# Kernel tuning notes

Hardware: AMD Instinct MI355X
Metric: run time of the kernel (lower is better)

## Reference

```python
import jax, jax.numpy as jnp
from jax import lax
import numpy as np

EPS_START, EPS_END, EPS_DECAY = 1.0, 0.05, 10000.0


def gru_step(x, h, w_ih, w_hh, b_ih, b_hh):
    # PyTorch GRUCell math; gates stacked as [r, z, n]
    gi = x @ w_ih.T + b_ih
    gh = h @ w_hh.T + b_hh
    i_r, i_z, i_n = jnp.split(gi, 3, axis=1)
    h_r, h_z, h_n = jnp.split(gh, 3, axis=1)
    r = jax.nn.sigmoid(i_r + h_r)
    z = jax.nn.sigmoid(i_z + h_z)
    n = jnp.tanh(i_n + r * h_n)
    return (1.0 - z) * n + z * h


def setup_inputs() -> dict:
    key = jax.random.key(0)
    ks = jax.random.split(key, 7)
    V, E, H = 32000, 256, 512
    s = 0.05
    return {
        "embedding": jax.random.normal(ks[0], (V, E), jnp.float32) * s,
        "w_ih": jax.random.normal(ks[1], (3 * H, E), jnp.float32) * s,
        "w_hh": jax.random.normal(ks[2], (3 * H, H), jnp.float32) * s,
        "b_ih": jax.random.normal(ks[3], (3 * H,), jnp.float32) * s,
        "b_hh": jax.random.normal(ks[4], (3 * H,), jnp.float32) * s,
        "w_out": jax.random.normal(ks[5], (V, H), jnp.float32) * s,
        "b_out": jax.random.normal(ks[6], (V,), jnp.float32) * s,
        "seq_len": 256,
        "batch_size": 512,
    }


def reference(embedding, w_ih, w_hh, b_ih, b_hh, w_out, b_out, seq_len, batch_size):
    V, E = embedding.shape
    H = w_hh.shape[1]
    B = batch_size
    log_unif = jnp.float32(np.log(V))  # -log(vocab_size) fill for epsilon-greedy

    keys = jax.random.split(jax.random.key(42), seq_len)
    ts = jnp.arange(seq_len, dtype=jnp.float32)

    h0 = jnp.zeros((B, H), jnp.float32)
    x0 = jnp.broadcast_to(embedding[0], (B, E))  # start token id 0

    def step(carry, inp):
        h, x = carry
        t, k = inp
        k_eps, k_gum = jax.random.split(k)
        h = gru_step(x, h, w_ih, w_hh, b_ih, b_hh)
        logp = jax.nn.log_softmax(h @ w_out.T + b_out, axis=1)  # [B, V]
        eps_t = EPS_END + (EPS_START - EPS_END) * jnp.exp(-4.0 * t / EPS_DECAY)
        draw = eps_t >= jax.random.uniform(k_eps, (B,))
        masked = jnp.where(draw[:, None], -log_unif, logp)
        g = jax.random.gumbel(k_gum, (B, V), jnp.float32)
        sampled = jnp.argmax(masked + g, axis=1)  # [B] int
        lp = jnp.take_along_axis(logp, sampled[:, None], axis=1)[:, 0]
        x_next = embedding[sampled]
        return (h, x_next), (sampled, lp)

    _, (samples, lps) = lax.scan(step, (h0, x0), (ts, keys))
    return samples.T, lps.T  # [B, S] each
```

## Files before the change

### kernel.cpp

```cpp
#include <hip/hip_runtime.h>
#include <math.h>
#include <stdio.h>

#ifndef JAX_PARTITIONABLE
#define JAX_PARTITIONABLE 1
#endif

namespace {

constexpr int B  = 512;
constexpr int S  = 256;
constexpr int E  = 256;
constexpr int H  = 512;
constexpr int V  = 32000;
constexpr int G3 = 3 * H;
constexpr int VBLK = 64;
constexpr int NCH  = V / VBLK;
constexpr int NDMAX = 96;

typedef __bf16 bf16x8 __attribute__((ext_vector_type(8)));
typedef float  f32x4  __attribute__((ext_vector_type(4)));
typedef unsigned u32x4 __attribute__((ext_vector_type(4)));

__device__ __forceinline__ void tf2x32(unsigned k0, unsigned k1,
                                       unsigned x0, unsigned x1,
                                       unsigned& o0, unsigned& o1) {
  unsigned ks2 = k0 ^ k1 ^ 0x1BD11BDAu;
  x0 += k0; x1 += k1;
#define TFR(r) { x0 += x1; x1 = (x1 << (r)) | (x1 >> (32 - (r))); x1 ^= x0; }
  TFR(13) TFR(15) TFR(26) TFR(6)   x0 += k1;  x1 += ks2 + 1u;
  TFR(17) TFR(29) TFR(16) TFR(24)  x0 += ks2; x1 += k0 + 2u;
  TFR(13) TFR(15) TFR(26) TFR(6)   x0 += k0;  x1 += k1 + 3u;
  TFR(17) TFR(29) TFR(16) TFR(24)  x0 += k1;  x1 += ks2 + 4u;
  TFR(13) TFR(15) TFR(26) TFR(6)   x0 += ks2; x1 += k0 + 5u;
#undef TFR
  o0 = x0; o1 = x1;
}

__device__ __forceinline__ unsigned rbits(unsigned g0, unsigned g1,
                                          unsigned b, unsigned v) {
#if JAX_PARTITIONABLE
  unsigned y0, y1;
  tf2x32(g0, g1, 0u, b * (unsigned)V + v, y0, y1);
  return y0 ^ y1;
#else
  const unsigned N2 = (unsigned)(B/2) * (unsigned)V;
  unsigned ii = b * (unsigned)V + v;
  unsigned jj = (b < 256) ? ii : ii - N2;
  unsigned y0, y1;
  tf2x32(g0, g1, jj, N2 + jj, y0, y1);
  return (b < 256) ? y0 : y1;
#endif
}

__device__ __forceinline__ float u01_from_bits(unsigned bits) {
  return __uint_as_float(0x3f800000u | (bits >> 9)) - 1.0f;
}

__device__ __forceinline__ float gumbel_exact(unsigned bits) {
  float u = u01_from_bits(bits);
  if (u == 0.0f) u = 1.1754943508222875e-38f;
  float w = (float)(-log((double)u));
  return (float)(-log((double)w));
}

__device__ __forceinline__ float gumbel_fast(unsigned bits) {
  float u = u01_from_bits(bits);
  if (u == 0.0f) u = 1.1754943508222875e-38f;
  float w = -__logf(u);
  return -__logf(w);
}

__device__ __forceinline__ unsigned short f2bf(float f) {
  unsigned u = __float_as_uint(f);
  unsigned r = (u + 0x7fffu + ((u >> 16) & 1u)) >> 16;
  return (unsigned short)r;
}

__device__ __forceinline__ size_t frag_off(int row, int k, int kTiles) {
  return ((size_t)((row >> 4) * kTiles + (k >> 5)) * 64
          + (row & 15) + 16 * ((k >> 3) & 3)) * 8 + (k & 7);
}

__global__ void k_init_rng(unsigned* __restrict__ kq, unsigned* __restrict__ ke) {
  int t = threadIdx.x;
  unsigned h0, h1, e0, e1, g0, g1;
#if JAX_PARTITIONABLE
  tf2x32(0u, 42u, 0u, (unsigned)t, h0, h1);
  tf2x32(h0, h1, 0u, 0u, e0, e1);
  tf2x32(h0, h1, 0u, 1u, g0, g1);
#else
  unsigned a0, a1, b0, b1;
  if (t < 128) {
    tf2x32(0u, 42u, (unsigned)(2*t),   (unsigned)(256+2*t), a0, a1);
    tf2x32(0u, 42u, (unsigned)(2*t+1), (unsigned)(257+2*t), b0, b1);
    h0 = a0; h1 = b0;
  } else {
    int j = 2*t - 256;
    tf2x32(0u, 42u, (unsigned)j,     (unsigned)(256+j), a0, a1);
    tf2x32(0u, 42u, (unsigned)(j+1), (unsigned)(257+j), b0, b1);
    h0 = a1; h1 = b1;
  }
  unsigned p0, p1, q0, q1;
  tf2x32(h0, h1, 0u, 2u, p0, p1);
  tf2x32(h0, h1, 1u, 3u, q0, q1);
  e0 = p0; e1 = q0; g0 = p1; g1 = q1;
#endif
  ke[2*t] = e0; ke[2*t+1] = e1;
  kq[2*t] = g0; kq[2*t+1] = g1;
}

__global__ void k_init_draws(const unsigned* __restrict__ ke,
                             unsigned char* __restrict__ draws) {
  int t = blockIdx.x;
  int b = threadIdx.x;
  unsigned k0 = ke[2*t], k1 = ke[2*t+1];
  unsigned bits, y0, y1;
#if JAX_PARTITIONABLE
  tf2x32(k0, k1, 0u, (unsigned)b, y0, y1);
  bits = y0 ^ y1;
#else
  if (b < 256) { tf2x32(k0, k1, (unsigned)b,       (unsigned)(256+b), y0, y1); bits = y0; }
  else         { tf2x32(k0, k1, (unsigned)(b-256), (unsigned)b,       y0, y1); bits = y1; }
#endif
  float u   = u01_from_bits(bits);
  float tf  = (float)t;
  float ex  = expf(__fmul_rn(-4.0f, tf) / 10000.0f);
  float eps = __fadd_rn(0.05f, __fmul_rn(0.95f, ex));
  draws[t*B + b] = (eps >= u) ? 1 : 0;
}

__global__ void k_init_nd(const unsigned char* __restrict__ draws,
                          int* __restrict__ nd_slot) {
  int t = blockIdx.x;
  if (threadIdx.x != 0) return;
  int cnt = 0;
  for (int b = 0; b < B; b++) {
    if (!draws[t*B + b] && cnt < NDMAX) nd_slot[t*B + b] = cnt++;
    else nd_slot[t*B + b] = -1;
  }
}

__global__ __launch_bounds__(256) void k_pre_argmax(
    const unsigned* __restrict__ kq, const unsigned char* __restrict__ draws,
    int* __restrict__ pre) {
  const int job  = blockIdx.x * 4 + (threadIdx.x >> 6);
  const int lane = threadIdx.x & 63;
  const int t = job >> 9, b = job & (B - 1);
  if (!draws[t*B + b]) { if (lane == 0) pre[job] = -1; return; }
  const unsigned g0 = kq[2*t], g1 = kq[2*t+1];
  unsigned best = 0u; int bv = V;
  for (int v = lane; v < V; v += 64) {
    unsigned bits = rbits(g0, g1, (unsigned)b, (unsigned)v) >> 9;
    if (bits > best || (bits == best && v < bv)) { best = bits; bv = v; }
  }
#pragma unroll
  for (int m = 1; m < 64; m <<= 1) {
    unsigned ob = __shfl_xor(best, m, 64);
    int      ov = __shfl_xor(bv,   m, 64);
    if (ob > best || (ob == best && ov < bv)) { best = ob; bv = ov; }
  }
  if (lane == 0) pre[job] = bv;
}

__global__ void k_init_state(float* __restrict__ h, int* __restrict__ samp) {
  int b = blockIdx.x, tid = threadIdx.x;
  h[b*H + tid] = 0.0f;
  h[b*H + 256 + tid] = 0.0f;
  if (tid == 0) samp[b] = 0;
}

__global__ void k_cast_w(const float* __restrict__ w,
                         unsigned short* __restrict__ w_sw) {
  int g = blockIdx.x*256 + threadIdx.x;
  int v  = g >> 6;
  int k0 = (g & 63) * 8;
  const float* src = w + (size_t)v*H + k0;
  union { unsigned short s[8]; u32x4 vv; } u;
#pragma unroll
  for (int e = 0; e < 8; e++) u.s[e] = f2bf(src[e]);
  *(u32x4*)&w_sw[frag_off(v, k0, H/32)] = u.vv;
}

__global__ __launch_bounds__(512) void k_emb_gates(
    const float* __restrict__ emb, const float* __restrict__ w_ih,
    const float* __restrict__ b_ih, float* __restrict__ EG) {
  __shared__ __align__(16) float As[16][68];
  __shared__ __align__(16) float Ws[16][68];
  const int tid = threadIdx.x;
  const int tx = tid & 15, ty = tid >> 4;
  const int row0 = blockIdx.y * 64, col0 = blockIdx.x * 64;
  float acc[2][4] = {};
  for (int k0 = 0; k0 < E; k0 += 16) {
#pragma unroll
    for (int l = 0; l < 2; l++) {
      int idx = tid + l*512;
      int r = idx >> 4, kk = idx & 15;
      As[kk][r] = emb[(size_t)(row0 + r)*E + k0 + kk];
      Ws[kk][r] = w_ih[(size_t)(col0 + r)*E + k0 + kk];
    }
    __syncthreads();
#pragma unroll
    for (int kk = 0; kk < 16; kk++) {
      const float2 av = *(const float2*)&As[kk][ty*2];
      const float4 wv = *(const float4*)&Ws[kk][tx*4];
      const float a[2] = {av.x, av.y};
      const float w[4] = {wv.x, wv.y, wv.z, wv.w};
#pragma unroll
      for (int i = 0; i < 2; i++)
#pragma unroll
        for (int j = 0; j < 4; j++) acc[i][j] = fmaf(a[i], w[j], acc[i][j]);
    }
    __syncthreads();
  }
#pragma unroll
  for (int i = 0; i < 2; i++) {
    int r = row0 + ty*2 + i;
    int c = col0 + tx*4;
    float4 o;
    o.x = __fadd_rn(acc[i][0], b_ih[c + 0]);
    o.y = __fadd_rn(acc[i][1], b_ih[c + 1]);
    o.z = __fadd_rn(acc[i][2], b_ih[c + 2]);
    o.w = __fadd_rn(acc[i][3], b_ih[c + 3]);
    *(float4*)&EG[(size_t)r*G3 + c] = o;
  }
}

__device__ __forceinline__ float sigm_acc(float v) {
  return (float)(1.0 / (1.0 + exp(-(double)v)));
}
__device__ __forceinline__ float tanh_acc(float v) {
  return (float)tanh((double)v);
}

__global__ __launch_bounds__(256) void k_gates_finish(
    const float* __restrict__ h, const float* __restrict__ w_hh,
    const float* __restrict__ b_hh, float* __restrict__ gh,
    const float* __restrict__ pmax, const float* __restrict__ psum,
    const float* __restrict__ plog,
    int* __restrict__ pre, const int* __restrict__ nd_slot,
    const float* __restrict__ nd_keys, const float* __restrict__ nd_kmax,
    const unsigned* __restrict__ kq, const unsigned char* __restrict__ draws,
    const float* __restrict__ w_out, const float* __restrict__ b_out,
    float* __restrict__ out_samples, float* __restrict__ out_lps,
    int* __restrict__ samp, int t) {
  const int tid = threadIdx.x;
  union Sh {
    struct { float As[2][16][68]; float Ws[2][16][52]; } g;
    struct { float sA[256]; int cand[160]; float ck[160]; float cl[160];
             int ccnt; int samp; float blog; } f;
    struct { unsigned sb[4]; int sv[4]; } p;
  };
  __shared__ Sh sh;

  if (blockIdx.x < 256) {
    if (t >= S) return;
    const int jw = tid & 15, rg = tid >> 4;
    const int j0 = (blockIdx.x & 31) * 16;
    const int row0 = (blockIdx.x >> 5) * 64;
    float ah[4][3] = {};
    float pa[4], pw[3];
#pragma unroll
    for (int l = 0; l < 4; l++) {
      int idx = tid + l*256;
      pa[l] = h[(size_t)(row0 + (idx >> 4))*H + (idx & 15)];
    }
#pragma unroll
    for (int l = 0; l < 3; l++) {
      int idx = tid + l*256;
      int c = idx >> 4;
      pw[l] = w_hh[(size_t)((c >> 4)*512 + j0 + (c & 15))*H + (idx & 15)];
    }
#pragma unroll
    for (int l = 0; l < 4; l++) {
      int idx = tid + l*256;
      sh.g.As[0][idx & 15][idx >> 4] = pa[l];
    }
#pragma unroll
    for (int l = 0; l < 3; l++) {
      int idx = tid + l*256;
      sh.g.Ws[0][idx & 15][idx >> 4] = pw[l];
    }
    __syncthreads();
    int p = 0;
#pragma unroll 1
    for (int tile = 0; tile < 32; tile++) {
      if (tile < 31) {
        const int k0 = (tile + 1) * 16;
#pragma unroll
        for (int l = 0; l < 4; l++) {
          int idx = tid + l*256;
          pa[l] = h[(size_t)(row0 + (idx >> 4))*H + k0 + (idx & 15)];
        }
#pragma unroll
        for (int l = 0; l < 3; l++) {
          int idx = tid + l*256;
          int c = idx >> 4;
          pw[l] = w_hh[(size_t)((c >> 4)*512 + j0 + (c & 15))*H + k0 + (idx & 15)];
        }
      }
#pragma unroll
      for (int kk = 0; kk < 16; kk++) {
        const float4 av = *(const float4*)&sh.g.As[p][kk][rg*4];
        const float a[4] = {av.x, av.y, av.z, av.w};
        const float w0 = sh.g.Ws[p][kk][jw];
        const float w1 = sh.g.Ws[p][kk][16 + jw];
        const float w2 = sh.g.Ws[p][kk][32 + jw];
#pragma unroll
        for (int i = 0; i < 4; i++) {
          ah[i][0] = fmaf(a[i], w0, ah[i][0]);
          ah[i][1] = fmaf(a[i], w1, ah[i][1]);
          ah[i][2] = fmaf(a[i], w2, ah[i][2]);
        }
      }
      if (tile < 31) {
#pragma unroll
        for (int l = 0; l < 4; l++) {
          int idx = tid + l*256;
          sh.g.As[p ^ 1][idx & 15][idx >> 4] = pa[l];
        }
#pragma unroll
        for (int l = 0; l < 3; l++) {
          int idx = tid + l*256;
          sh.g.Ws[p ^ 1][idx & 15][idx >> 4] = pw[l];
        }
        __syncthreads();
        p ^= 1;
      }
    }
    const int j = j0 + jw;
    const float bh_r = b_hh[j], bh_z = b_hh[512 + j], bh_n = b_hh[1024 + j];
#pragma unroll
    for (int i = 0; i < 4; i++) {
      const int b = row0 + rg*4 + i;
      gh[(size_t)b*G3 +        j] = __fadd_rn(ah[i][0], bh_r);
      gh[(size_t)b*G3 +  512 + j] = __fadd_rn(ah[i][1], bh_z);
      gh[(size_t)b*G3 + 1024 + j] = __fadd_rn(ah[i][2], bh_n);
    }
    return;
  }

  if (blockIdx.x >= 768) {
    const int tn = t + 1;
    if (tn >= S) return;
    const int b = blockIdx.x - 768;
    if (!draws[tn*B + b]) { if (tid == 0) pre[tn*B + b] = -1; return; }
    const unsigned g0 = kq[2*tn], g1 = kq[2*tn+1];
    unsigned best = 0u; int bv = V;
    for (int v = tid; v < V; v += 256) {
      unsigned bits = rbits(g0, g1, (unsigned)b, (unsigned)v) >> 9;
      if (bits > best || (bits == best && v < bv)) { best = bits; bv = v; }
    }
#pragma unroll
    for (int m = 1; m < 64; m <<= 1) {
      unsigned ob = __shfl_xor(best, m, 64);
      int      ov = __shfl_xor(bv,   m, 64);
      if (ob > best || (ob == best && ov < bv)) { best = ob; bv = ov; }
    }
    const int wv = tid >> 6;
    if ((tid & 63) == 0) { sh.p.sb[wv] = best; sh.p.sv[wv] = bv; }
    __syncthreads();
    if (tid == 0) {
      for (int i = 1; i < 4; i++) {
        unsigned ob = sh.p.sb[i]; int ov = sh.p.sv[i];
        if (ob > best || (ob == best && ov < bv)) { best = ob; bv = ov; }
      }
      pre[tn*B + b] = bv;
    }
    return;
  }

  const int tf = t - 1;
  if (tf < 0) return;
  const int b = blockIdx.x - 256;
  const int* pre_t     = pre + tf*B;
  const int* nd_slot_t = nd_slot + tf*B;

  float m = -INFINITY;
  for (int c = tid; c < NCH; c += 256) m = fmaxf(m, pmax[b*NCH + c]);
  sh.f.sA[tid] = m; __syncthreads();
  for (int s = 128; s > 0; s >>= 1) {
    if (tid < s) sh.f.sA[tid] = fmaxf(sh.f.sA[tid], sh.f.sA[tid+s]);
    __syncthreads();
  }
  const float M = sh.f.sA[0];
  __syncthreads();
  float sum = 0.0f;
  for (int c = tid; c < NCH; c += 256)
    sum += psum[b*NCH + c] * expf(pmax[b*NCH + c] - M);
  sh.f.sA[tid] = sum; __syncthreads();
  for (int s = 128; s > 0; s >>= 1) {
    if (tid < s) sh.f.sA[tid] += sh.f.sA[tid+s];
    __syncthreads();
  }
  const float SUM = sh.f.sA[0];
  __syncthreads();

  const int pr = pre_t[b];
  if (pr >= 0) {
    if (tid == 0) { sh.f.samp = pr; sh.f.blog = plog[b]; }
  } else {
    const int slot = nd_slot_t[b];
    if (slot < 0) {
      if (tid == 0) { sh.f.samp = 0; sh.f.blog = plog[b]; }
    } else {
      const unsigned g0 = kq[2*tf], g1 = kq[2*tf+1];
      if (tid == 0) sh.f.ccnt = 0;
      float km = -INFINITY;
      for (int c = tid; c < NCH; c += 256) km = fmaxf(km, nd_kmax[slot*NCH + c]);
      sh.f.sA[tid] = km; __syncthreads();
      for (int s = 128; s > 0; s >>= 1) {
        if (tid < s) sh.f.sA[tid] = fmaxf(sh.f.sA[tid], sh.f.sA[tid+s]);
        __syncthreads();
      }
      const float thr = sh.f.sA[0] - 0.0859375f;
      __syncthreads();
      const float* keys = nd_keys + (size_t)slot*V;
      for (int c = tid; c < NCH; c += 256) {
        if (nd_kmax[slot*NCH + c] >= thr) {
          for (int j = 0; j < VBLK; j++) {
            float k = keys[c*VBLK + j];
            if (k >= thr) {
              int p = atomicAdd(&sh.f.ccnt, 1);
              if (p < 160) sh.f.cand[p] = c*VBLK + j;
            }
          }
        }
      }
      __syncthreads();
      const int nc = min(sh.f.ccnt, 160);
      const int wid = tid >> 6, lane = tid & 63;
      for (int c = wid; c < nc; c += 4) {
        const int v = sh.f.cand[c];
        const float* wr = w_out + (size_t)v*H;
        const float* hr = h + (size_t)b*H;
        float s = 0.0f;
#pragma unroll
        for (int i = 0; i < 8; i++) s = fmaf(hr[lane + 64*i], wr[lane + 64*i], s);
#pragma unroll
        for (int mm = 1; mm < 64; mm <<= 1) s += __shfl_xor(s, mm, 64);
        if (lane == 0) {
          float logit = __fadd_rn(s, b_out[v]);
          float key   = __fadd_rn(logit,
                          gumbel_exact(rbits(g0, g1, (unsigned)b, (unsigned)v)));
          sh.f.ck[c] = key; sh.f.cl[c] = logit;
        }
      }
      __syncthreads();
      if (tid == 0) {
        float bk = -INFINITY; int bv = V; float bl = 0.0f;
        for (int c = 0; c < nc; c++) {
          float k = sh.f.ck[c]; int v = sh.f.cand[c];
          if (k > bk || (k == bk && v < bv)) { bk = k; bv = v; bl = sh.f.cl[c]; }
        }
        sh.f.samp = bv; sh.f.blog = bl;
      }
    }
  }
  __syncthreads();
  if (tid == 0) {
    const int sampled = sh.f.samp;
    float lse = (float)log((double)SUM);
    float lp  = __fsub_rn(__fsub_rn(sh.f.blog, M), lse);
    out_samples[b*S + tf] = (float)sampled;
    out_lps[b*S + tf]     = lp;
    samp[b] = sampled;
  }
}

__global__ void k_gru(const float* __restrict__ EG, const int* __restrict__ samp,
                      const float* __restrict__ gh, float* __restrict__ h,
                      unsigned short* __restrict__ h_sw) {
  int g = blockIdx.x*256 + threadIdx.x;
  int b  = g >> 6;
  int j0 = (g & 63) * 8;
  const float* gib = EG + (size_t)samp[b]*G3;
  const float* ghb = gh + (size_t)b*G3;
  float hn[8];
  union { unsigned short s[8]; u32x4 vv; } u;
#pragma unroll
  for (int e = 0; e < 8; e++) {
    int j = j0 + e;
    float r  = sigm_acc(__fadd_rn(gib[j],     ghb[j]));
    float zz = sigm_acc(__fadd_rn(gib[H+j],   ghb[H+j]));
    float nn = tanh_acc(__fadd_rn(gib[2*H+j], __fmul_rn(r, ghb[2*H+j])));
    float hv = h[(size_t)b*H + j];
    float t1 = __fmul_rn(__fsub_rn(1.0f, zz), nn);
    float t2 = __fmul_rn(zz, hv);
    hn[e] = __fadd_rn(t1, t2);
    u.s[e] = f2bf(hn[e]);
  }
#pragma unroll
  for (int e = 0; e < 8; e++) h[(size_t)b*H + j0 + e] = hn[e];
  *(u32x4*)&h_sw[frag_off(b, j0, H/32)] = u.vv;
}

__global__ __launch_bounds__(256) void k_xgru(
    const float* __restrict__ emb, const int* __restrict__ samp,
    const float* __restrict__ w_ih, const float* __restrict__ b_ih,
    const float* __restrict__ gh, float* __restrict__ h,
    unsigned short* __restrict__ h_sw) {
  __shared__ __align__(16) float As[2][16][68];
  __shared__ __align__(16) float Ws[2][16][52];
  __shared__ int srow[64];
  const int tid = threadIdx.x;
  const int jw = tid & 15, rg = tid >> 4;
  const int j0 = blockIdx.x * 16;
  const int row0 = blockIdx.y * 64;
  if (tid < 64) srow[tid] = samp[row0 + tid];
  __syncthreads();

  float ai[4][3] = {};
  float pa[4], pw[3];
#pragma unroll
  for (int l = 0; l < 4; l++) {
    int idx = tid + l*256;
    pa[l] = emb[(size_t)srow[idx >> 4]*E + (idx & 15)];
  }
#pragma unroll
  for (int l = 0; l < 3; l++) {
    int idx = tid + l*256;
    int c = idx >> 4;
    pw[l] = w_ih[(size_t)((c >> 4)*512 + j0 + (c & 15))*E + (idx & 15)];
  }
#pragma unroll
  for (int l = 0; l < 4; l++) {
    int idx = tid + l*256;
    As[0][idx & 15][idx >> 4] = pa[l];
  }
#pragma unroll
  for (int l = 0; l < 3; l++) {
    int idx = tid + l*256;
    Ws[0][idx & 15][idx >> 4] = pw[l];
  }
  __syncthreads();
  int p = 0;
#pragma unroll 1
  for (int tile = 0; tile < 16; tile++) {
    if (tile < 15) {
      const int k0 = (tile + 1) * 16;
#pragma unroll
      for (int l = 0; l < 4; l++) {
        int idx = tid + l*256;
        pa[l] = emb[(size_t)srow[idx >> 4]*E + k0 + (idx & 15)];
      }
#pragma unroll
      for (int l = 0; l < 3; l++) {
        int idx = tid + l*256;
        int c = idx >> 4;
        pw[l] = w_ih[(size_t)((c >> 4)*512 + j0 + (c & 15))*E + k0 + (idx & 15)];
      }
    }
#pragma unroll
    for (int kk = 0; kk < 16; kk++) {
      const float4 av = *(const float4*)&As[p][kk][rg*4];
      const float a[4] = {av.x, av.y, av.z, av.w};
      const float w0 = Ws[p][kk][jw];
      const float w1 = Ws[p][kk][16 + jw];
      const float w2 = Ws[p][kk][32 + jw];
#pragma unroll
      for (int i = 0; i < 4; i++) {
        ai[i][0] = fmaf(a[i], w0, ai[i][0]);
        ai[i][1] = fmaf(a[i], w1, ai[i][1]);
        ai[i][2] = fmaf(a[i], w2, ai[i][2]);
      }
    }
    if (tile < 15) {
#pragma unroll
      for (int l = 0; l < 4; l++) {
        int idx = tid + l*256;
        As[p ^ 1][idx & 15][idx >> 4] = pa[l];
      }
#pragma unroll
      for (int l = 0; l < 3; l++) {
        int idx = tid + l*256;
        Ws[p ^ 1][idx & 15][idx >> 4] = pw[l];
      }
      __syncthreads();
      p ^= 1;
    }
  }

  const int j = j0 + jw;
  const float bi_r = b_ih[j], bi_z = b_ih[512 + j], bi_n = b_ih[1024 + j];
#pragma unroll
  for (int i = 0; i < 4; i++) {
    const int b = row0 + rg*4 + i;
    float gi_r = __fadd_rn(ai[i][0], bi_r);
    float gi_z = __fadd_rn(ai[i][1], bi_z);
    float gi_n = __fadd_rn(ai[i][2], bi_n);
    float gh_r = gh[(size_t)b*G3 + j];
    float gh_z = gh[(size_t)b*G3 + 512 + j];
    float gh_n = gh[(size_t)b*G3 + 1024 + j];
    float r  = sigm_acc(__fadd_rn(gi_r, gh_r));
    float zz = sigm_acc(__fadd_rn(gi_z, gh_z));
    float nn = tanh_acc(__fadd_rn(gi_n, __fmul_rn(r, gh_n)));
    float hv = h[(size_t)b*H + j];
    float t1 = __fmul_rn(__fsub_rn(1.0f, zz), nn);
    float t2 = __fmul_rn(zz, hv);
    float hn = __fadd_rn(t1, t2);
    h[(size_t)b*H + j] = hn;
    h_sw[frag_off(b, j, H/32)] = f2bf(hn);
  }
}

__global__ __launch_bounds__(256) void k_mfma_logits(
    const unsigned short* __restrict__ h_sw,
    const unsigned short* __restrict__ w_sw,
    const float* __restrict__ b_out,
    const unsigned* __restrict__ kq,
    const int* __restrict__ pre_t,
    const int* __restrict__ nd_slot_t,
    float* __restrict__ pmax, float* __restrict__ psum,
    float* __restrict__ plog,
    float* __restrict__ nd_keys, float* __restrict__ nd_kmax, int t) {
  const int tid  = threadIdx.x;

  const int L  = blockIdx.y * 512 + blockIdx.x;
  const int wg = (L & 7) * 128 + (L >> 3);
  if (wg >= 2*NCH) return;
  const int vblk = wg >> 1;
  const int bblk = wg & 1;
  const int lane = tid & 63, w = tid >> 6;
  const int quad = lane >> 4, l15 = lane & 15;

  f32x4 acc[4][4] = {};

  const int mtBase = bblk*16 + w*4;
  const int ntBase = vblk*4;
  const unsigned short* hp = h_sw + (size_t)mtBase*16*512 + lane*8;
  const unsigned short* wp = w_sw + (size_t)ntBase*16*512 + lane*8;

  bf16x8 afc[4], bfc[4];
#pragma unroll
  for (int mt = 0; mt < 4; mt++)
    afc[mt] = __builtin_bit_cast(bf16x8, *(const u32x4*)(hp + (size_t)(mt*16)*512));
#pragma unroll
  for (int nt = 0; nt < 4; nt++)
    bfc[nt] = __builtin_bit_cast(bf16x8, *(const u32x4*)(wp + (size_t)(nt*16)*512));

#pragma unroll 1
  for (int kt = 0; kt < 15; kt++) {
    bf16x8 afn[4], bfn[4];
#pragma unroll
    for (int mt = 0; mt < 4; mt++)
      afn[mt] = __builtin_bit_cast(bf16x8,
          *(const u32x4*)(hp + (size_t)(mt*16 + kt + 1)*512));
#pragma unroll
    for (int nt = 0; nt < 4; nt++)
      bfn[nt] = __builtin_bit_cast(bf16x8,
          *(const u32x4*)(wp + (size_t)(nt*16 + kt + 1)*512));
#pragma unroll
    for (int mt = 0; mt < 4; mt++)
#pragma unroll
      for (int nt = 0; nt < 4; nt++)
        acc[mt][nt] = __builtin_amdgcn_mfma_f32_16x16x32_bf16(
            afc[mt], bfc[nt], acc[mt][nt], 0, 0, 0);
#pragma unroll
    for (int mt = 0; mt < 4; mt++) afc[mt] = afn[mt];
#pragma unroll
    for (int nt = 0; nt < 4; nt++) bfc[nt] = bfn[nt];
  }
  {
#pragma unroll
    for (int mt = 0; mt < 4; mt++)
#pragma unroll
      for (int nt = 0; nt < 4; nt++)
        acc[mt][nt] = __builtin_amdgcn_mfma_f32_16x16x32_bf16(
            afc[mt], bfc[nt], acc[mt][nt], 0, 0, 0);
  }

  const int bW = bblk*256 + w*64;
  const int vW = vblk*64;
  const unsigned g0 = kq[2*t], g1 = kq[2*t+1];
  float bias[4];
#pragma unroll
  for (int nt = 0; nt < 4; nt++) bias[nt] = b_out[vW + nt*16 + l15];

#pragma unroll
  for (int mt = 0; mt < 4; mt++) {
#pragma unroll
    for (int r = 0; r < 4; r++) {
      const int b = bW + mt*16 + quad*4 + r;
      float lg[4];
#pragma unroll
      for (int nt = 0; nt < 4; nt++) lg[nt] = acc[mt][nt][r] + bias[nt];
      float lmax = fmaxf(fmaxf(lg[0], lg[1]), fmaxf(lg[2], lg[3]));
#pragma unroll
      for (int m = 1; m < 16; m <<= 1) lmax = fmaxf(lmax, __shfl_xor(lmax, m, 64));
      float ls = 0.0f;
#pragma unroll
      for (int nt = 0; nt < 4; nt++) ls += __expf(lg[nt] - lmax);
#pragma unroll
      for (int m = 1; m < 16; m <<= 1) ls += __shfl_xor(ls, m, 64);
      if (l15 == 0) { pmax[b*NCH + vblk] = lmax; psum[b*NCH + vblk] = ls; }
      const int pr = pre_t[b];
      if (pr >= 0) {
        int rel = pr - vW;
        if (rel >= 0 && rel < 64 && (rel & 15) == l15) plog[b] = lg[rel >> 4];
      } else {
        const int slot = nd_slot_t[b];
        if (slot >= 0) {
          float key[4];
#pragma unroll
          for (int nt = 0; nt < 4; nt++)
            key[nt] = lg[nt] + gumbel_fast(
                rbits(g0, g1, (unsigned)b, (unsigned)(vW + nt*16 + l15)));
          float* dst = nd_keys + (size_t)slot*V + vW + l15;
#pragma unroll
          for (int nt = 0; nt < 4; nt++) dst[nt*16] = key[nt];
          float kmx = fmaxf(fmaxf(key[0], key[1]), fmaxf(key[2], key[3]));
#pragma unroll
          for (int m = 1; m < 16; m <<= 1) kmx = fmaxf(kmx, __shfl_xor(kmx, m, 64));
          if (l15 == 0) nd_kmax[slot*NCH + vblk] = kmx;
        }
      }
    }
  }
}

}

extern "C" void kernel_launch(void* const* d_in, const int* in_sizes, int n_in,
                              void* d_out, int out_size, void* d_ws, size_t ws_size,
                              hipStream_t stream) {
  (void)in_sizes; (void)n_in; (void)out_size;
  const float* emb   = (const float*)d_in[0];
  const float* w_ih  = (const float*)d_in[1];
  const float* w_hh  = (const float*)d_in[2];
  const float* b_ih  = (const float*)d_in[3];
  const float* b_hh  = (const float*)d_in[4];
  const float* w_out = (const float*)d_in[5];
  const float* b_out = (const float*)d_in[6];
  float* out = (float*)d_out;

  char* wsb = (char*)d_ws;
  size_t off = 0;
  auto alloc = [&](size_t nbytes) {
    char* p = wsb + off;
    off += (nbytes + 255) & ~size_t(255);
    return p;
  };
  float* h     = (float*)alloc((size_t)B*H*4);
  float* gh    = (float*)alloc((size_t)B*G3*4);
  unsigned short* h_sw = (unsigned short*)alloc((size_t)B*H*2);
  unsigned short* w_sw = (unsigned short*)alloc((size_t)V*H*2);
  float* pmax  = (float*)alloc((size_t)B*NCH*4);
  float* psum  = (float*)alloc((size_t)B*NCH*4);
  float* plog  = (float*)alloc((size_t)B*4);
  unsigned* kq = (unsigned*)alloc((size_t)S*2*4);
  unsigned* ke = (unsigned*)alloc((size_t)S*2*4);
  unsigned char* draws = (unsigned char*)alloc((size_t)S*B);
  int* pre     = (int*)alloc((size_t)S*B*4);
  int* nd_slot = (int*)alloc((size_t)S*B*4);
  float* nd_keys = (float*)alloc((size_t)NDMAX*V*4);
  float* nd_kmax = (float*)alloc((size_t)NDMAX*NCH*4);
  int* samp    = (int*)alloc((size_t)B*4);
  if (off > ws_size) {
    fprintf(stderr, "kernel_launch: workspace too small (need %zu, have %zu)\n",
            off, ws_size);
    return;
  }
  const size_t eg_bytes = ((size_t)V*G3*4 + 255) & ~size_t(255);
  const bool use_eg = (off + eg_bytes <= ws_size);
  float* EG = use_eg ? (float*)alloc(eg_bytes) : nullptr;

  k_init_rng<<<1, S, 0, stream>>>(kq, ke);
  k_init_draws<<<S, B, 0, stream>>>(ke, draws);
  k_init_nd<<<S, 64, 0, stream>>>(draws, nd_slot);
  k_pre_argmax<<<B/4, 256, 0, stream>>>(kq, draws, pre);
  k_init_state<<<B, 256, 0, stream>>>(h, samp);
  k_cast_w<<<(V*H/8)/256, 256, 0, stream>>>(w_out, w_sw);
  if (use_eg)
    k_emb_gates<<<dim3(G3/64, V/64), 512, 0, stream>>>(emb, w_ih, b_ih, EG);

  for (int t = 0; t < S; t++) {
    k_gates_finish<<<1280, 256, 0, stream>>>(
        h, w_hh, b_hh, gh, pmax, psum, plog, pre, nd_slot,
        nd_keys, nd_kmax, kq, draws, w_out, b_out,
        out, out + (size_t)B*S, samp, t);
    if (use_eg)
      k_gru<<<(B*H/8)/256, 256, 0, stream>>>(EG, samp, gh, h, h_sw);
    else
      k_xgru<<<dim3(32, 8), 256, 0, stream>>>(emb, samp, w_ih, b_ih,
                                              gh, h, h_sw);
    k_mfma_logits<<<dim3(512, 2), 256, 0, stream>>>(
        h_sw, w_sw, b_out, kq, pre + t*B, nd_slot + t*B,
        pmax, psum, plog, nd_keys, nd_kmax, t);
  }
  k_gates_finish<<<1280, 256, 0, stream>>>(
      h, w_hh, b_hh, gh, pmax, psum, plog, pre, nd_slot,
      nd_keys, nd_kmax, kq, draws, w_out, b_out,
      out, out + (size_t)B*S, samp, S);
}
```

Baseline: 33.87 ms.

## Fuse sampling finish with GRU update and overlap hidden-gate GEMM with logits

Each step goes from three launches to two on the embedding-gate path. The new k_fingru combines finishing the previous step's sample with the GRU update. The recurrent h@w_hh GEMM for the next step now runs in extra blocks of the logits MFMA kernel, so it overlaps the output projection. The epsilon-branch argmax precompute is also moved from one upfront kernel into extra blocks of k_fingru. The aim is to cut per-step launch overhead and serial dependency, in exchange for more complex block-role dispatch, and gh is initialised to b_hh.

```diff
diff --git a/kernel.cpp b/kernel.cpp
--- a/kernel.cpp
+++ b/kernel.cpp
@@ -163,11 +163,15 @@
   if (lane == 0) pre[job] = bv;
 }
 
-__global__ void k_init_state(float* __restrict__ h, int* __restrict__ samp) {
+__global__ void k_init_state(float* __restrict__ h, int* __restrict__ samp,
+                             float* __restrict__ gh,
+                             const float* __restrict__ b_hh) {
   int b = blockIdx.x, tid = threadIdx.x;
   h[b*H + tid] = 0.0f;
   h[b*H + 256 + tid] = 0.0f;
   if (tid == 0) samp[b] = 0;
+#pragma unroll
+  for (int i = 0; i < 6; i++) gh[(size_t)b*G3 + i*256 + tid] = b_hh[i*256 + tid];
 }
 
 __global__ void k_cast_w(const float* __restrict__ w,
@@ -231,6 +235,382 @@
 }
 __device__ __forceinline__ float tanh_acc(float v) {
   return (float)tanh((double)v);
+}
+
+__global__ __launch_bounds__(256) void k_fingru(
+    const float* __restrict__ EG, const float* __restrict__ gh,
+    float* __restrict__ h, unsigned short* __restrict__ h_sw,
+    const float* __restrict__ pmax, const float* __restrict__ psum,
+    const float* __restrict__ plog,
+    int* __restrict__ pre, const int* __restrict__ nd_slot,
+    const float* __restrict__ nd_keys, const float* __restrict__ nd_kmax,
+    const unsigned* __restrict__ kq, const unsigned char* __restrict__ draws,
+    const float* __restrict__ w_out, const float* __restrict__ b_out,
+    float* __restrict__ out_samples, float* __restrict__ out_lps,
+    int* __restrict__ samp, int t) {
+  const int tid = threadIdx.x;
+
+  if (blockIdx.x >= 512) {
+    __shared__ unsigned sb[4];
+    __shared__ int      sv[4];
+    if (t >= S) return;
+    const int b = blockIdx.x - 512;
+    if (!draws[t*B + b]) { if (tid == 0) pre[t*B + b] = -1; return; }
+    const unsigned g0 = kq[2*t], g1 = kq[2*t+1];
+    unsigned best = 0u; int bv = V;
+    for (int v = tid; v < V; v += 256) {
+      unsigned bits = rbits(g0, g1, (unsigned)b, (unsigned)v) >> 9;
+      if (bits > best || (bits == best && v < bv)) { best = bits; bv = v; }
+    }
+#pragma unroll
+    for (int m = 1; m < 64; m <<= 1) {
+      unsigned ob = __shfl_xor(best, m, 64);
+      int      ov = __shfl_xor(bv,   m, 64);
+      if (ob > best || (ob == best && ov < bv)) { best = ob; bv = ov; }
+    }
+    const int wv = tid >> 6;
+    if ((tid & 63) == 0) { sb[wv] = best; sv[wv] = bv; }
+    __syncthreads();
+    if (tid == 0) {
+      for (int i = 1; i < 4; i++) {
+        unsigned ob = sb[i]; int ov = sv[i];
+        if (ob > best || (ob == best && ov < bv)) { best = ob; bv = ov; }
+      }
+      pre[t*B + b] = bv;
+    }
+    return;
+  }
+
+  const int b = blockIdx.x;
+  __shared__ float sA[256];
+  __shared__ int   cand[160];
+  __shared__ float cand_key[160], cand_lg[160];
+  __shared__ int   ccnt;
+  __shared__ int   s_samp;
+  __shared__ float s_blog;
+
+  const int tf = t - 1;
+  if (tf >= 0) {
+    const int* pre_t     = pre + tf*B;
+    const int* nd_slot_t = nd_slot + tf*B;
+
+    float m = -INFINITY;
+    for (int c = tid; c < NCH; c += 256) m = fmaxf(m, pmax[b*NCH + c]);
+    sA[tid] = m; __syncthreads();
+    for (int s = 128; s > 0; s >>= 1) {
+      if (tid < s) sA[tid] = fmaxf(sA[tid], sA[tid+s]);
+      __syncthreads();
+    }
+    const float M = sA[0];
+    __syncthreads();
+    float sum = 0.0f;
+    for (int c = tid; c < NCH; c += 256)
+      sum += psum[b*NCH + c] * expf(pmax[b*NCH + c] - M);
+    sA[tid] = sum; __syncthreads();
+    for (int s = 128; s > 0; s >>= 1) {
+      if (tid < s) sA[tid] += sA[tid+s];
+      __syncthreads();
+    }
+    const float SUM = sA[0];
+    __syncthreads();
+
+    const int pr = pre_t[b];
+    if (pr >= 0) {
+      if (tid == 0) { s_samp = pr; s_blog = plog[b]; }
+    } else {
+      const int slot = nd_slot_t[b];
+      if (slot < 0) {
+        if (tid == 0) { s_samp = 0; s_blog = plog[b]; }
+      } else {
+        const unsigned g0 = kq[2*tf], g1 = kq[2*tf+1];
+        if (tid == 0) ccnt = 0;
+        float km = -INFINITY;
+        for (int c = tid; c < NCH; c += 256) km = fmaxf(km, nd_kmax[slot*NCH + c]);
+        sA[tid] = km; __syncthreads();
+        for (int s = 128; s > 0; s >>= 1) {
+          if (tid < s) sA[tid] = fmaxf(sA[tid], sA[tid+s]);
+          __syncthreads();
+        }
+        const float thr = sA[0] - 0.0859375f;
+        __syncthreads();
+        const float* keys = nd_keys + (size_t)slot*V;
+        for (int c = tid; c < NCH; c += 256) {
+          if (nd_kmax[slot*NCH + c] >= thr) {
+            for (int j = 0; j < VBLK; j++) {
+              float k = keys[c*VBLK + j];
+              if (k >= thr) {
+                int p = atomicAdd(&ccnt, 1);
+                if (p < 160) cand[p] = c*VBLK + j;
+              }
+            }
+          }
+        }
+        __syncthreads();
+        const int nc = min(ccnt, 160);
+        const int wid = tid >> 6, lane = tid & 63;
+        for (int c = wid; c < nc; c += 4) {
+          const int v = cand[c];
+          const float* wr = w_out + (size_t)v*H;
+          const float* hr = h + (size_t)b*H;
+          float s = 0.0f;
+#pragma unroll
+          for (int i = 0; i < 8; i++) s = fmaf(hr[lane + 64*i], wr[lane + 64*i], s);
+#pragma unroll
+          for (int mm = 1; mm < 64; mm <<= 1) s += __shfl_xor(s, mm, 64);
+          if (lane == 0) {
+            float logit = __fadd_rn(s, b_out[v]);
+            float key   = __fadd_rn(logit,
+                            gumbel_exact(rbits(g0, g1, (unsigned)b, (unsigned)v)));
+            cand_key[c] = key; cand_lg[c] = logit;
+          }
+        }
+        __syncthreads();
+        if (tid == 0) {
+          float bk = -INFINITY; int bv = V; float bl = 0.0f;
+          for (int c = 0; c < nc; c++) {
+            float k = cand_key[c]; int v = cand[c];
+            if (k > bk || (k == bk && v < bv)) { bk = k; bv = v; bl = cand_lg[c]; }
+          }
+          s_samp = bv; s_blog = bl;
+        }
+      }
+    }
+    __syncthreads();
+    if (tid == 0) {
+      const int sampled = s_samp;
+      float lse = (float)log((double)SUM);
+      float lp  = __fsub_rn(__fsub_rn(s_blog, M), lse);
+      out_samples[b*S + tf] = (float)sampled;
+      out_lps[b*S + tf]     = lp;
+      samp[b] = sampled;
+    }
+    __syncthreads();
+  }
+
+  if (t >= S) return;
+  const int smp = (tf >= 0) ? s_samp : samp[b];
+
+  const float* gib = EG + (size_t)smp*G3;
+  const float* ghb = gh + (size_t)b*G3;
+#pragma unroll
+  for (int e = 0; e < 2; e++) {
+    const int j = tid*2 + e;
+    float r  = sigm_acc(__fadd_rn(gib[j],     ghb[j]));
+    float zz = sigm_acc(__fadd_rn(gib[H+j],   ghb[H+j]));
+    float nn = tanh_acc(__fadd_rn(gib[2*H+j], __fmul_rn(r, ghb[2*H+j])));
+    float hv = h[(size_t)b*H + j];
+    float t1 = __fmul_rn(__fsub_rn(1.0f, zz), nn);
+    float t2 = __fmul_rn(zz, hv);
+    float hn = __fadd_rn(t1, t2);
+    h[(size_t)b*H + j] = hn;
+    h_sw[frag_off(b, j, H/32)] = f2bf(hn);
+  }
+}
+
+__global__ __launch_bounds__(256) void k_mfma_logits(
+    const unsigned short* __restrict__ h_sw,
+    const unsigned short* __restrict__ w_sw,
+    const float* __restrict__ b_out,
+    const unsigned* __restrict__ kq,
+    const int* __restrict__ pre_t,
+    const int* __restrict__ nd_slot_t,
+    float* __restrict__ pmax, float* __restrict__ psum,
+    float* __restrict__ plog,
+    float* __restrict__ nd_keys, float* __restrict__ nd_kmax,
+    const float* __restrict__ h, const float* __restrict__ w_hh,
+    const float* __restrict__ b_hh, float* __restrict__ gh, int t) {
+  const int tid  = threadIdx.x;
+  __shared__ __align__(16) float As[2][16][68];
+  __shared__ __align__(16) float Ws[2][16][52];
+
+  if (blockIdx.x >= 1024) {
+    const int sb = blockIdx.x - 1024;
+    const int jw = tid & 15, rg = tid >> 4;
+    const int j0 = (sb & 31) * 16;
+    const int row0 = (sb >> 5) * 64;
+    float ah[4][3] = {};
+    float pa[4], pw[3];
+#pragma unroll
+    for (int l = 0; l < 4; l++) {
+      int idx = tid + l*256;
+      pa[l] = h[(size_t)(row0 + (idx >> 4))*H + (idx & 15)];
+    }
+#pragma unroll
+    for (int l = 0; l < 3; l++) {
+      int idx = tid + l*256;
+      int c = idx >> 4;
+      pw[l] = w_hh[(size_t)((c >> 4)*512 + j0 + (c & 15))*H + (idx & 15)];
+    }
+#pragma unroll
+    for (int l = 0; l < 4; l++) {
+      int idx = tid + l*256;
+      As[0][idx & 15][idx >> 4] = pa[l];
+    }
+#pragma unroll
+    for (int l = 0; l < 3; l++) {
+      int idx = tid + l*256;
+      Ws[0][idx & 15][idx >> 4] = pw[l];
+    }
+    __syncthreads();
+    int p = 0;
+#pragma unroll 1
+    for (int tile = 0; tile < 32; tile++) {
+      if (tile < 31) {
+        const int k0 = (tile + 1) * 16;
+#pragma unroll
+        for (int l = 0; l < 4; l++) {
+          int idx = tid + l*256;
+          pa[l] = h[(size_t)(row0 + (idx >> 4))*H + k0 + (idx & 15)];
+        }
+#pragma unroll
+        for (int l = 0; l < 3; l++) {
+          int idx = tid + l*256;
+          int c = idx >> 4;
+          pw[l] = w_hh[(size_t)((c >> 4)*512 + j0 + (c & 15))*H + k0 + (idx & 15)];
+        }
+      }
+#pragma unroll
+      for (int kk = 0; kk < 16; kk++) {
+        const float4 av = *(const float4*)&As[p][kk][rg*4];
+        const float a[4] = {av.x, av.y, av.z, av.w};
+        const float w0 = Ws[p][kk][jw];
+        const float w1 = Ws[p][kk][16 + jw];
+        const float w2 = Ws[p][kk][32 + jw];
+#pragma unroll
+        for (int i = 0; i < 4; i++) {
+          ah[i][0] = fmaf(a[i], w0, ah[i][0]);
+          ah[i][1] = fmaf(a[i], w1, ah[i][1]);
+          ah[i][2] = fmaf(a[i], w2, ah[i][2]);
+        }
+      }
+      if (tile < 31) {
+#pragma unroll
+        for (int l = 0; l < 4; l++) {
+          int idx = tid + l*256;
+          As[p ^ 1][idx & 15][idx >> 4] = pa[l];
+        }
+#pragma unroll
+        for (int l = 0; l < 3; l++) {
+          int idx = tid + l*256;
+          Ws[p ^ 1][idx & 15][idx >> 4] = pw[l];
+        }
+        __syncthreads();
+        p ^= 1;
+      }
+    }
+    const int j = j0 + jw;
+    const float bh_r = b_hh[j], bh_z = b_hh[512 + j], bh_n = b_hh[1024 + j];
+#pragma unroll
+    for (int i = 0; i < 4; i++) {
+      const int b = row0 + rg*4 + i;
+      gh[(size_t)b*G3 +        j] = __fadd_rn(ah[i][0], bh_r);
+      gh[(size_t)b*G3 +  512 + j] = __fadd_rn(ah[i][1], bh_z);
+      gh[(size_t)b*G3 + 1024 + j] = __fadd_rn(ah[i][2], bh_n);
+    }
+    return;
+  }
+
+  const int L  = blockIdx.x;
+  const int wg = (L & 7) * 128 + (L >> 3);
+  if (wg >= 2*NCH) return;
+  const int vblk = wg >> 1;
+  const int bblk = wg & 1;
+  const int lane = tid & 63, w = tid >> 6;
+  const int quad = lane >> 4, l15 = lane & 15;
+
+  f32x4 acc[4][4] = {};
+
+  const int mtBase = bblk*16 + w*4;
+  const int ntBase = vblk*4;
+  const unsigned short* hp = h_sw + (size_t)mtBase*16*512 + lane*8;
+  const unsigned short* wp = w_sw + (size_t)ntBase*16*512 + lane*8;
+
+  bf16x8 afc[4], bfc[4];
+#pragma unroll
+  for (int mt = 0; mt < 4; mt++)
+    afc[mt] = __builtin_bit_cast(bf16x8, *(const u32x4*)(hp + (size_t)(mt*16)*512));
+#pragma unroll
+  for (int nt = 0; nt < 4; nt++)
+    bfc[nt] = __builtin_bit_cast(bf16x8, *(const u32x4*)(wp + (size_t)(nt*16)*512));
+
+#pragma unroll 1
+  for (int kt = 0; kt < 15; kt++) {
+    bf16x8 afn[4], bfn[4];
+#pragma unroll
+    for (int mt = 0; mt < 4; mt++)
+      afn[mt] = __builtin_bit_cast(bf16x8,
+          *(const u32x4*)(hp + (size_t)(mt*16 + kt + 1)*512));
+#pragma unroll
+    for (int nt = 0; nt < 4; nt++)
+      bfn[nt] = __builtin_bit_cast(bf16x8,
+          *(const u32x4*)(wp + (size_t)(nt*16 + kt + 1)*512));
+#pragma unroll
+    for (int mt = 0; mt < 4; mt++)
+#pragma unroll
+      for (int nt = 0; nt < 4; nt++)
+        acc[mt][nt] = __builtin_amdgcn_mfma_f32_16x16x32_bf16(
+            afc[mt], bfc[nt], acc[mt][nt], 0, 0, 0);
+#pragma unroll
+    for (int mt = 0; mt < 4; mt++) afc[mt] = afn[mt];
+#pragma unroll
+    for (int nt = 0; nt < 4; nt++) bfc[nt] = bfn[nt];
+  }
+  {
+#pragma unroll
+    for (int mt = 0; mt < 4; mt++)
+#pragma unroll
+      for (int nt = 0; nt < 4; nt++)
+        acc[mt][nt] = __builtin_amdgcn_mfma_f32_16x16x32_bf16(
+            afc[mt], bfc[nt], acc[mt][nt], 0, 0, 0);
+  }
+
+  const int bW = bblk*256 + w*64;
+  const int vW = vblk*64;
+  const unsigned g0 = kq[2*t], g1 = kq[2*t+1];
+  float bias[4];
+#pragma unroll
+  for (int nt = 0; nt < 4; nt++) bias[nt] = b_out[vW + nt*16 + l15];
+
+#pragma unroll
+  for (int mt = 0; mt < 4; mt++) {
+#pragma unroll
+    for (int r = 0; r < 4; r++) {
+      const int b = bW + mt*16 + quad*4 + r;
+      float lg[4];
+#pragma unroll
+      for (int nt = 0; nt < 4; nt++) lg[nt] = acc[mt][nt][r] + bias[nt];
+      float lmax = fmaxf(fmaxf(lg[0], lg[1]), fmaxf(lg[2], lg[3]));
+#pragma unroll
+      for (int m = 1; m < 16; m <<= 1) lmax = fmaxf(lmax, __shfl_xor(lmax, m, 64));
+      float ls = 0.0f;
+#pragma unroll
+      for (int nt = 0; nt < 4; nt++) ls += __expf(lg[nt] - lmax);
+#pragma unroll
+      for (int m = 1; m < 16; m <<= 1) ls += __shfl_xor(ls, m, 64);
+      if (l15 == 0) { pmax[b*NCH + vblk] = lmax; psum[b*NCH + vblk] = ls; }
+      const int pr = pre_t[b];
+      if (pr >= 0) {
+        int rel = pr - vW;
+        if (rel >= 0 && rel < 64 && (rel & 15) == l15) plog[b] = lg[rel >> 4];
+      } else {
+        const int slot = nd_slot_t[b];
+        if (slot >= 0) {
+          float key[4];
+#pragma unroll
+          for (int nt = 0; nt < 4; nt++)
+            key[nt] = lg[nt] + gumbel_fast(
+                rbits(g0, g1, (unsigned)b, (unsigned)(vW + nt*16 + l15)));
+          float* dst = nd_keys + (size_t)slot*V + vW + l15;
+#pragma unroll
+          for (int nt = 0; nt < 4; nt++) dst[nt*16] = key[nt];
+          float kmx = fmaxf(fmaxf(key[0], key[1]), fmaxf(key[2], key[3]));
+#pragma unroll
+          for (int m = 1; m < 16; m <<= 1) kmx = fmaxf(kmx, __shfl_xor(kmx, m, 64));
+          if (l15 == 0) nd_kmax[slot*NCH + vblk] = kmx;
+        }
+      }
+    }
+  }
 }
 
 __global__ __launch_bounds__(256) void k_gates_finish(
@@ -468,33 +848,6 @@
   }
 }
 
-__global__ void k_gru(const float* __restrict__ EG, const int* __restrict__ samp,
-                      const float* __restrict__ gh, float* __restrict__ h,
-                      unsigned short* __restrict__ h_sw) {
-  int g = blockIdx.x*256 + threadIdx.x;
-  int b  = g >> 6;
-  int j0 = (g & 63) * 8;
-  const float* gib = EG + (size_t)samp[b]*G3;
-  const float* ghb = gh + (size_t)b*G3;
-  float hn[8];
-  union { unsigned short s[8]; u32x4 vv; } u;
-#pragma unroll
-  for (int e = 0; e < 8; e++) {
-    int j = j0 + e;
-    float r  = sigm_acc(__fadd_rn(gib[j],     ghb[j]));
-    float zz = sigm_acc(__fadd_rn(gib[H+j],   ghb[H+j]));
-    float nn = tanh_acc(__fadd_rn(gib[2*H+j], __fmul_rn(r, ghb[2*H+j])));
-    float hv = h[(size_t)b*H + j];
-    float t1 = __fmul_rn(__fsub_rn(1.0f, zz), nn);
-    float t2 = __fmul_rn(zz, hv);
-    hn[e] = __fadd_rn(t1, t2);
-    u.s[e] = f2bf(hn[e]);
-  }
-#pragma unroll
-  for (int e = 0; e < 8; e++) h[(size_t)b*H + j0 + e] = hn[e];
-  *(u32x4*)&h_sw[frag_off(b, j0, H/32)] = u.vv;
-}
-
 __global__ __launch_bounds__(256) void k_xgru(
     const float* __restrict__ emb, const int* __restrict__ samp,
     const float* __restrict__ w_ih, const float* __restrict__ b_ih,
@@ -601,121 +954,6 @@
     float hn = __fadd_rn(t1, t2);
     h[(size_t)b*H + j] = hn;
     h_sw[frag_off(b, j, H/32)] = f2bf(hn);
-  }
-}
-
-__global__ __launch_bounds__(256) void k_mfma_logits(
-    const unsigned short* __restrict__ h_sw,
-    const unsigned short* __restrict__ w_sw,
-    const float* __restrict__ b_out,
-    const unsigned* __restrict__ kq,
-    const int* __restrict__ pre_t,
-    const int* __restrict__ nd_slot_t,
-    float* __restrict__ pmax, float* __restrict__ psum,
-    float* __restrict__ plog,
-    float* __restrict__ nd_keys, float* __restrict__ nd_kmax, int t) {
-  const int tid  = threadIdx.x;
-
-  const int L  = blockIdx.y * 512 + blockIdx.x;
-  const int wg = (L & 7) * 128 + (L >> 3);
-  if (wg >= 2*NCH) return;
-  const int vblk = wg >> 1;
-  const int bblk = wg & 1;
-  const int lane = tid & 63, w = tid >> 6;
-  const int quad = lane >> 4, l15 = lane & 15;
-
-  f32x4 acc[4][4] = {};
-
-  const int mtBase = bblk*16 + w*4;
-  const int ntBase = vblk*4;
-  const unsigned short* hp = h_sw + (size_t)mtBase*16*512 + lane*8;
-  const unsigned short* wp = w_sw + (size_t)ntBase*16*512 + lane*8;
-
-  bf16x8 afc[4], bfc[4];
-#pragma unroll
-  for (int mt = 0; mt < 4; mt++)
-    afc[mt] = __builtin_bit_cast(bf16x8, *(const u32x4*)(hp + (size_t)(mt*16)*512));
-#pragma unroll
-  for (int nt = 0; nt < 4; nt++)
-    bfc[nt] = __builtin_bit_cast(bf16x8, *(const u32x4*)(wp + (size_t)(nt*16)*512));
-
-#pragma unroll 1
-  for (int kt = 0; kt < 15; kt++) {
-    bf16x8 afn[4], bfn[4];
-#pragma unroll
-    for (int mt = 0; mt < 4; mt++)
-      afn[mt] = __builtin_bit_cast(bf16x8,
-          *(const u32x4*)(hp + (size_t)(mt*16 + kt + 1)*512));
-#pragma unroll
-    for (int nt = 0; nt < 4; nt++)
-      bfn[nt] = __builtin_bit_cast(bf16x8,
-          *(const u32x4*)(wp + (size_t)(nt*16 + kt + 1)*512));
-#pragma unroll
-    for (int mt = 0; mt < 4; mt++)
-#pragma unroll
-      for (int nt = 0; nt < 4; nt++)
-        acc[mt][nt] = __builtin_amdgcn_mfma_f32_16x16x32_bf16(
-            afc[mt], bfc[nt], acc[mt][nt], 0, 0, 0);
-#pragma unroll
-    for (int mt = 0; mt < 4; mt++) afc[mt] = afn[mt];
-#pragma unroll
-    for (int nt = 0; nt < 4; nt++) bfc[nt] = bfn[nt];
-  }
-  {
-#pragma unroll
-    for (int mt = 0; mt < 4; mt++)
-#pragma unroll
-      for (int nt = 0; nt < 4; nt++)
-        acc[mt][nt] = __builtin_amdgcn_mfma_f32_16x16x32_bf16(
-            afc[mt], bfc[nt], acc[mt][nt], 0, 0, 0);
-  }
-
-  const int bW = bblk*256 + w*64;
-  const int vW = vblk*64;
-  const unsigned g0 = kq[2*t], g1 = kq[2*t+1];
-  float bias[4];
-#pragma unroll
-  for (int nt = 0; nt < 4; nt++) bias[nt] = b_out[vW + nt*16 + l15];
-
-#pragma unroll
-  for (int mt = 0; mt < 4; mt++) {
-#pragma unroll
-    for (int r = 0; r < 4; r++) {
-      const int b = bW + mt*16 + quad*4 + r;
-      float lg[4];
-#pragma unroll
-      for (int nt = 0; nt < 4; nt++) lg[nt] = acc[mt][nt][r] + bias[nt];
-      float lmax = fmaxf(fmaxf(lg[0], lg[1]), fmaxf(lg[2], lg[3]));
-#pragma unroll
-      for (int m = 1; m < 16; m <<= 1) lmax = fmaxf(lmax, __shfl_xor(lmax, m, 64));
-      float ls = 0.0f;
-#pragma unroll
-      for (int nt = 0; nt < 4; nt++) ls += __expf(lg[nt] - lmax);
-#pragma unroll
-      for (int m = 1; m < 16; m <<= 1) ls += __shfl_xor(ls, m, 64);
-      if (l15 == 0) { pmax[b*NCH + vblk] = lmax; psum[b*NCH + vblk] = ls; }
-      const int pr = pre_t[b];
-      if (pr >= 0) {
-        int rel = pr - vW;
-        if (rel >= 0 && rel < 64 && (rel & 15) == l15) plog[b] = lg[rel >> 4];
-      } else {
-        const int slot = nd_slot_t[b];
-        if (slot >= 0) {
-          float key[4];
-#pragma unroll
-          for (int nt = 0; nt < 4; nt++)
-            key[nt] = lg[nt] + gumbel_fast(
-                rbits(g0, g1, (unsigned)b, (unsigned)(vW + nt*16 + l15)));
-          float* dst = nd_keys + (size_t)slot*V + vW + l15;
-#pragma unroll
-          for (int nt = 0; nt < 4; nt++) dst[nt*16] = key[nt];
-          float kmx = fmaxf(fmaxf(key[0], key[1]), fmaxf(key[2], key[3]));
-#pragma unroll
-          for (int m = 1; m < 16; m <<= 1) kmx = fmaxf(kmx, __shfl_xor(kmx, m, 64));
-          if (l15 == 0) nd_kmax[slot*NCH + vblk] = kmx;
-        }
-      }
-    }
   }
 }
 
@@ -768,28 +1006,40 @@
   k_init_rng<<<1, S, 0, stream>>>(kq, ke);
   k_init_draws<<<S, B, 0, stream>>>(ke, draws);
   k_init_nd<<<S, 64, 0, stream>>>(draws, nd_slot);
-  k_pre_argmax<<<B/4, 256, 0, stream>>>(kq, draws, pre);
-  k_init_state<<<B, 256, 0, stream>>>(h, samp);
+  k_init_state<<<B, 256, 0, stream>>>(h, samp, gh, b_hh);
   k_cast_w<<<(V*H/8)/256, 256, 0, stream>>>(w_out, w_sw);
-  if (use_eg)
+
+  if (use_eg) {
     k_emb_gates<<<dim3(G3/64, V/64), 512, 0, stream>>>(emb, w_ih, b_ih, EG);
-
-  for (int t = 0; t < S; t++) {
+    for (int t = 0; t < S; t++) {
+      k_fingru<<<1024, 256, 0, stream>>>(
+          EG, gh, h, h_sw, pmax, psum, plog, pre, nd_slot,
+          nd_keys, nd_kmax, kq, draws, w_out, b_out,
+          out, out + (size_t)B*S, samp, t);
+      k_mfma_logits<<<1280, 256, 0, stream>>>(
+          h_sw, w_sw, b_out, kq, pre + t*B, nd_slot + t*B,
+          pmax, psum, plog, nd_keys, nd_kmax, h, w_hh, b_hh, gh, t);
+    }
+    k_fingru<<<1024, 256, 0, stream>>>(
+        EG, gh, h, h_sw, pmax, psum, plog, pre, nd_slot,
+        nd_keys, nd_kmax, kq, draws, w_out, b_out,
+        out, out + (size_t)B*S, samp, S);
+  } else {
+    k_pre_argmax<<<B/4, 256, 0, stream>>>(kq, draws, pre);
+    for (int t = 0; t < S; t++) {
+      k_gates_finish<<<1280, 256, 0, stream>>>(
+          h, w_hh, b_hh, gh, pmax, psum, plog, pre, nd_slot,
+          nd_keys, nd_kmax, kq, draws, w_out, b_out,
+          out, out + (size_t)B*S, samp, t);
+      k_xgru<<<dim3(32, 8), 256, 0, stream>>>(emb, samp, w_ih, b_ih,
+                                              gh, h, h_sw);
+      k_mfma_logits<<<1024, 256, 0, stream>>>(
+          h_sw, w_sw, b_out, kq, pre + t*B, nd_slot + t*B,
+          pmax, psum, plog, nd_keys, nd_kmax, h, w_hh, b_hh, gh, t);
+    }
     k_gates_finish<<<1280, 256, 0, stream>>>(
         h, w_hh, b_hh, gh, pmax, psum, plog, pre, nd_slot,
         nd_keys, nd_kmax, kq, draws, w_out, b_out,
-        out, out + (size_t)B*S, samp, t);
-    if (use_eg)
-      k_gru<<<(B*H/8)/256, 256, 0, stream>>>(EG, samp, gh, h, h_sw);
-    else
-      k_xgru<<<dim3(32, 8), 256, 0, stream>>>(emb, samp, w_ih, b_ih,
-                                              gh, h, h_sw);
-    k_mfma_logits<<<dim3(512, 2), 256, 0, stream>>>(
-        h_sw, w_sw, b_out, kq, pre + t*B, nd_slot + t*B,
-        pmax, psum, plog, nd_keys, nd_kmax, t);
-  }
-  k_gates_finish<<<1280, 256, 0, stream>>>(
-      h, w_hh, b_hh, gh, pmax, psum, plog, pre, nd_slot,
-      nd_keys, nd_kmax, kq, draws, w_out, b_out,
-      out, out + (size_t)B*S, samp, S);
-}
+        out, out + (size_t)B*S, samp, S);
+  }
+}
```

After: 32.95 ms. 1.03x faster.
